# Kernel tuning notes

Hardware: AMD Instinct MI355X
Metric: run time of the kernel (lower is better)

Reference implementation:

```python
import jax, jax.numpy as jnp
import numpy as np

B, N, CIN, D, K = 8, 4096, 128, 128, 16
EPS = 1e-5


def setup_inputs() -> dict:
    key = jax.random.key(0)
    ks = jax.random.split(key, 16)
    g = lambda i, shp, s=0.05: (jax.random.normal(ks[i], shp, jnp.float32) * s)
    return {
        "xyz": jax.random.normal(ks[0], (B, N, 3), jnp.float32),
        "features": jax.random.normal(ks[1], (B, N, CIN), jnp.float32),
        # feature_transform: Linear(CIN->D) + LayerNorm(D)
        "W1": g(2, (CIN, D)), "b1": jnp.zeros((D,), jnp.float32),
        "ln1_g": jnp.ones((D,), jnp.float32), "ln1_b": jnp.zeros((D,), jnp.float32),
        # geo_encoder: Conv1d(3->D//2,1) + BN(D//2) + Conv1d(D//2->D,1)
        "cw1": g(3, (D // 2, 3), 0.3), "cb1": jnp.zeros((D // 2,), jnp.float32),
        "bn_g": jnp.ones((D // 2,), jnp.float32), "bn_b": jnp.zeros((D // 2,), jnp.float32),
        "cw2": g(4, (D, D // 2)), "cb2": jnp.zeros((D,), jnp.float32),
        # fusion: Linear(2D->D) + LayerNorm(D)
        "Wf": g(5, (2 * D, D)), "bf": jnp.zeros((D,), jnp.float32),
        "lnf_g": jnp.ones((D,), jnp.float32), "lnf_b": jnp.zeros((D,), jnp.float32),
        "alpha": jnp.ones((1, 1, D), jnp.float32), "beta": jnp.zeros((1, 1, D), jnp.float32),
    }


def _layernorm(x, g, b):
    m = x.mean(-1, keepdims=True)
    v = x.var(-1, keepdims=True)
    return (x - m) / jnp.sqrt(v + EPS) * g + b


def reference(xyz, features, W1, b1, ln1_g, ln1_b, cw1, cb1, bn_g, bn_b, cw2, cb2,
              Wf, bf, lnf_g, lnf_b, alpha, beta):
    # KNN via squared distances [B,N,N]
    sq = jnp.sum(xyz * xyz, -1)
    dist = sq[:, :, None] + sq[:, None, :] - 2.0 * jnp.einsum('bnc,bmc->bnm', xyz, xyz)
    _, idx = jax.lax.top_k(-dist, K)                       # [B,N,K] smallest dists

    gather = jax.vmap(lambda pts, i: pts[i])               # per-batch fancy gather
    nb_xyz = gather(xyz, idx)                              # [B,N,K,3]
    nb_feat = gather(features, idx)                        # [B,N,K,CIN]

    # geo encoder on relative positions (1x1 convs == per-point linear)
    rel = nb_xyz - xyz[:, :, None, :]                      # [B,N,K,3]
    h = jnp.einsum('bnkc,oc->bnko', rel, cw1) + cb1        # [B,N,K,D/2]
    mu = h.mean((0, 1, 2))                                 # BatchNorm1d (train-mode batch stats)
    var = h.var((0, 1, 2))
    h = (h - mu) / jnp.sqrt(var + EPS) * bn_g + bn_b
    h = jax.nn.silu(h)
    geo = jnp.einsum('bnkc,oc->bnko', h, cw2) + cb2        # [B,N,K,D]

    # feature transform on gathered neighbor features
    tf = jax.nn.silu(_layernorm(nb_feat @ W1 + b1, ln1_g, ln1_b))  # [B,N,K,D]

    # fuse, affine, softmax-weighted aggregation over K
    fused = jax.nn.silu(_layernorm(jnp.concatenate([tf, geo], -1) @ Wf + bf, lnf_g, lnf_b))
    fused = alpha * fused + beta                           # broadcast [1,1,D]
    w = jax.nn.softmax(fused.sum(-1), axis=-1)             # [B,N,K]
    return (w[..., None] * fused).sum(2)                   # [B,N,D]
```

## Files before the change

### kernel.cpp

```cpp
#include <hip/hip_runtime.h>
#include <hip/hip_bf16.h>

#define B_ 8
#define N_ 4096
#define K_ 16
#define D_ 128

typedef short bf16x8 __attribute__((ext_vector_type(8)));
typedef float f32x4 __attribute__((ext_vector_type(4)));

__device__ __forceinline__ short bfr(float x){
  __hip_bfloat16 h = __float2bfloat16(x);
  return *reinterpret_cast<short*>(&h);
}

__global__ __launch_bounds__(256) void prep_kernel(
    const float* __restrict__ W1, const float* __restrict__ Wf, const float* __restrict__ cw2,
    short* __restrict__ W1Tf, short* __restrict__ WfTf, short* __restrict__ cw2f,
    float* __restrict__ stats)
{
  int t = blockIdx.x*256 + threadIdx.x;
  if (t < 16384) {
    int u = t;
    int j = u & 7, L = (u >> 3) & 63, ks = (u >> 9) & 3, tt = u >> 11;
    int d = tt*16 + (L & 15);
    int c = ks*32 + (L >> 4)*8 + j;
    W1Tf[u] = bfr(W1[c*128 + d]);
  } else if (t < 49152) {
    int u = t - 16384;
    int j = u & 7, L = (u >> 3) & 63, ks = (u >> 9) & 7, tt = u >> 12;
    int d = tt*16 + (L & 15);
    int c = ks*32 + (L >> 4)*8 + j;
    WfTf[u] = bfr(Wf[c*128 + d]);
  } else if (t < 57344) {
    int u = t - 49152;
    int j = u & 7, L = (u >> 3) & 63, ks = (u >> 9) & 1, tt = u >> 10;
    int d = tt*16 + (L & 15);
    int c = ks*32 + (L >> 4)*8 + j;
    cw2f[u] = bfr(cw2[d*64 + c]);
  } else if (t < 57360) {
    stats[t - 57344] = 0.0f;
  }
}

__device__ __forceinline__ void insert16(float (&bd)[16], int (&bi)[16], float d, int cid){
  #pragma unroll
  for (int j = 15; j >= 1; --j){
    bool ltj = d < bd[j];
    bool ltp = d < bd[j-1];
    float nd = ltj ? (ltp ? bd[j-1] : d) : bd[j];
    int   ni = ltj ? (ltp ? bi[j-1] : cid) : bi[j];
    bd[j] = nd; bi[j] = ni;
  }
  bool lt0 = d < bd[0];
  bd[0] = lt0 ? d : bd[0];
  bi[0] = lt0 ? cid : bi[0];
}

__device__ __forceinline__ void insert16t(float (&bd)[16], int (&bi)[16], float d, int cid){
  bool lt[16];
  #pragma unroll
  for (int j = 0; j < 16; ++j)
    lt[j] = (d < bd[j]) || ((d == bd[j]) && (cid < bi[j]));
  #pragma unroll
  for (int j = 15; j >= 1; --j){
    float nd = lt[j] ? (lt[j-1] ? bd[j-1] : d) : bd[j];
    int   ni = lt[j] ? (lt[j-1] ? bi[j-1] : cid) : bi[j];
    bd[j] = nd; bi[j] = ni;
  }
  if (lt[0]){ bd[0] = d; bi[0] = cid; }
}

__global__ __launch_bounds__(512) void knn_split_kernel(
    const float* __restrict__ xyz,
    float* __restrict__ pd0, int* __restrict__ pi0,
    float* __restrict__ pd1, int* __restrict__ pi1)
{
  __shared__ float4 cand[2048];
  int b    = blockIdx.x >> 7;
  int h    = (blockIdx.x >> 6) & 1;
  int qblk = (blockIdx.x & 63) << 6;
  int hbase = h << 11;
  const float* xb = xyz + b*N_*3;
  for (int i = threadIdx.x; i < 2048; i += 512){
    int gi = hbase + i;
    float x = xb[gi*3+0], y = xb[gi*3+1], z = xb[gi*3+2];
    int e = i ^ ((i >> 8) & 7);
    cand[e] = make_float4(x, y, z, x*x + y*y + z*z);
  }
  __syncthreads();

  int wv = threadIdx.x >> 6, lane = threadIdx.x & 63;
  int q = lane & 7;
  int s = lane >> 3;
  int qi = qblk + (wv << 3) + q;
  const float* qp = xb + qi*3;
  float qx = qp[0], qy = qp[1], qz = qp[2];
  float4 qc = make_float4(qx, qy, qz, qx*qx + qy*qy + qz*qz);

  float bd[16]; int bi[16];
  #pragma unroll
  for (int j = 0; j < 16; ++j){ bd[j] = 3.4e38f; bi[j] = 0x7fffffff; }

  int cbase = s << 8;
  for (int m = 0; m < 256; ++m){
    float4 c = cand[cbase + (m ^ s)];
    float t = qc.x*c.x + qc.y*c.y + qc.z*c.z;
    float d = (qc.w + c.w) - 2.0f*t;
    if (d < bd[15]) insert16(bd, bi, d, cbase + m);
  }

  #pragma unroll
  for (int xm = 32; xm >= 8; xm >>= 1){
    bool absorb = (lane & xm) == 0;
    #pragma unroll
    for (int j = 0; j < 16; ++j){
      float pdj = __shfl_xor(bd[j], xm);
      int   pij = __shfl_xor(bi[j], xm);
      if (absorb) insert16t(bd, bi, pdj, pij);
    }
  }

  if (s == 0){
    int gq = b*N_ + qi;
    float* pdh = h ? pd1 : pd0;
    int*   pih = h ? pi1 : pi0;
    #pragma unroll
    for (int j = 0; j < 16; ++j){
      pdh[gq*16 + j] = bd[j];
      pih[gq*16 + j] = bi[j] + hbase;
    }
  }
}

__device__ __forceinline__ bool lexlt(float da, int ia, float db, int ib){
  return (da < db) || ((da == db) && (ia < ib));
}

__global__ __launch_bounds__(512) void knn_merge_kernel(
    const float* __restrict__ xyz,
    const float* __restrict__ pd0, const int* __restrict__ pi0,
    const float* __restrict__ pd1, const int* __restrict__ pi1,
    int* __restrict__ idx_out, float* __restrict__ stats)
{
  int gq = blockIdx.x*512 + threadIdx.x;
  int b = gq >> 12, qi = gq & 4095;

  float md[16]; int mi[16];
  #pragma unroll
  for (int i = 0; i < 16; ++i){
    float da = pd0[gq*16 + i];      int ia = pi0[gq*16 + i];
    float db = pd1[gq*16 + 15 - i]; int ib = pi1[gq*16 + 15 - i];
    bool t = lexlt(da, ia, db, ib);
    md[i] = t ? da : db; mi[i] = t ? ia : ib;
  }
  #pragma unroll
  for (int j = 8; j > 0; j >>= 1){
    #pragma unroll
    for (int i = 0; i < 16; ++i){
      int l = i ^ j;
      if (l > i){
        bool t = lexlt(md[l], mi[l], md[i], mi[i]);
        float lo_d = t ? md[l] : md[i]; int lo_i = t ? mi[l] : mi[i];
        float hi_d = t ? md[i] : md[l]; int hi_i = t ? mi[i] : mi[l];
        md[i] = lo_d; mi[i] = lo_i; md[l] = hi_d; mi[l] = hi_i;
      }
    }
  }

  const float* qp = xyz + (b*N_ + qi)*3;
  float qx = qp[0], qy = qp[1], qz = qp[2];
  float sv[9];
  #pragma unroll
  for (int i = 0; i < 9; ++i) sv[i] = 0.0f;
  #pragma unroll
  for (int j = 0; j < 16; ++j){
    idx_out[gq*16 + j] = mi[j];
    const float* np = xyz + (b*N_ + mi[j])*3;
    float rx = np[0]-qx, ry = np[1]-qy, rz = np[2]-qz;
    sv[0] += rx;    sv[1] += ry;    sv[2] += rz;
    sv[3] += rx*rx; sv[4] += ry*ry; sv[5] += rz*rz;
    sv[6] += rx*ry; sv[7] += rx*rz; sv[8] += ry*rz;
  }
  #pragma unroll
  for (int i = 0; i < 9; ++i){
    float v = sv[i];
    #pragma unroll
    for (int mask = 1; mask < 64; mask <<= 1) v += __shfl_xor(v, mask);
    if ((threadIdx.x & 63) == 0) atomicAdd(&stats[i], v);
  }
}

__global__ void bn_finalize_kernel(
    const float* __restrict__ stats, const float* __restrict__ cw1, const float* __restrict__ cb1,
    const float* __restrict__ bn_g, const float* __restrict__ bn_b,
    float* __restrict__ bnsc, float* __restrict__ bnsh)
{
  int o = threadIdx.x;
  if (o >= 64) return;
  const float inv = 1.0f / (float)(B_*N_*K_);
  float m1x = stats[0]*inv, m1y = stats[1]*inv, m1z = stats[2]*inv;
  float mxx = stats[3]*inv, myy = stats[4]*inv, mzz = stats[5]*inv;
  float mxy = stats[6]*inv, mxz = stats[7]*inv, myz = stats[8]*inv;
  float w0 = cw1[o*3], w1 = cw1[o*3+1], w2 = cw1[o*3+2], cb = cb1[o];
  float wm = w0*m1x + w1*m1y + w2*m1z;
  float mu = wm + cb;
  float e2 = w0*w0*mxx + w1*w1*myy + w2*w2*mzz
           + 2.0f*(w0*w1*mxy + w0*w2*mxz + w1*w2*myz)
           + 2.0f*cb*wm + cb*cb;
  float var = e2 - mu*mu;
  float sc = bn_g[o] * rsqrtf(var + 1e-5f);
  bnsc[o] = sc;
  bnsh[o] = bn_b[o] - mu*sc;
}

__device__ __forceinline__ void ln_silu_store(
    f32x4 (&acc)[8], const float (&pb)[8], const float (&pg)[8], const float (&pe)[8],
    short* fw, int g, int c16)
{
  float sm[4] = {0,0,0,0}, sq[4] = {0,0,0,0};
  #pragma unroll
  for (int t = 0; t < 8; ++t){
    #pragma unroll
    for (int r = 0; r < 4; ++r){
      float v = acc[t][r] + pb[t];
      acc[t][r] = v;
      sm[r] += v; sq[r] += v*v;
    }
  }
  #pragma unroll
  for (int mask = 1; mask < 16; mask <<= 1){
    #pragma unroll
    for (int r = 0; r < 4; ++r){ sm[r] += __shfl_xor(sm[r], mask); sq[r] += __shfl_xor(sq[r], mask); }
  }
  #pragma unroll
  for (int r = 0; r < 4; ++r){
    float mean = sm[r] * (1.0f/128.0f);
    float var  = sq[r]*(1.0f/128.0f) - mean*mean;
    float rstd = rsqrtf(var + 1e-5f);
    #pragma unroll
    for (int t = 0; t < 8; ++t){
      float y = (acc[t][r] - mean) * rstd * pg[t] + pe[t];
      y = y / (1.0f + __expf(-y));
      fw[(g*4 + r)*264 + t*16 + c16] = bfr(y);
    }
  }
}

__device__ __forceinline__ void geo_store(
    float rx, float ry, float rz,
    const float* s_cw1, const float* s_cb1, const float* s_sc, const float* s_sh,
    const short* __restrict__ cw2f, const float (&pc2)[8],
    short* fw, int g, int c16, int lane)
{
  bf16x8 a2[2];
  #pragma unroll
  for (int ks = 0; ks < 2; ++ks){
    bf16x8 v;
    #pragma unroll
    for (int j = 0; j < 8; ++j){
      int o = ks*32 + g*8 + j;
      float h = s_cw1[o*3]*rx + s_cw1[o*3+1]*ry + s_cw1[o*3+2]*rz + s_cb1[o];
      h = h * s_sc[o] + s_sh[o];
      h = h / (1.0f + __expf(-h));
      v[j] = bfr(h);
    }
    a2[ks] = v;
  }
  #pragma unroll
  for (int t = 0; t < 8; ++t){
    f32x4 a = (f32x4){0.f,0.f,0.f,0.f};
    #pragma unroll
    for (int ks = 0; ks < 2; ++ks){
      bf16x8 w = *(const bf16x8*)(cw2f + ((t*2 + ks)*64 + lane)*8);
      a = __builtin_amdgcn_mfma_f32_16x16x32_bf16(a2[ks], w, a, 0, 0, 0);
    }
    #pragma unroll
    for (int r = 0; r < 4; ++r)
      fw[(g*4 + r)*264 + 128 + t*16 + c16] = bfr(a[r] + pc2[t]);
  }
}

__device__ __forceinline__ void epilogue_store(
    f32x4 (&acc)[8], const float (&pbf)[8], const float (&pgf)[8], const float (&pef)[8],
    const float (&pal)[8], const float (&pbt)[8],
    int point, int g, int c16, float* __restrict__ out)
{
  float sm[4] = {0,0,0,0}, sq[4] = {0,0,0,0};
  #pragma unroll
  for (int t = 0; t < 8; ++t){
    #pragma unroll
    for (int r = 0; r < 4; ++r){
      float v = acc[t][r] + pbf[t];
      acc[t][r] = v;
      sm[r] += v; sq[r] += v*v;
    }
  }
  #pragma unroll
  for (int mask = 1; mask < 16; mask <<= 1){
    #pragma unroll
    for (int r = 0; r < 4; ++r){ sm[r] += __shfl_xor(sm[r], mask); sq[r] += __shfl_xor(sq[r], mask); }
  }
  #pragma unroll
  for (int r = 0; r < 4; ++r){
    float mean = sm[r] * (1.0f/128.0f);
    float var  = sq[r]*(1.0f/128.0f) - mean*mean;
    float rstd = rsqrtf(var + 1e-5f);
    #pragma unroll
    for (int t = 0; t < 8; ++t){
      float y = (acc[t][r] - mean) * rstd * pgf[t] + pef[t];
      y = y / (1.0f + __expf(-y));
      acc[t][r] = pal[t]*y + pbt[t];
    }
  }
  float sr[4] = {0,0,0,0};
  #pragma unroll
  for (int t = 0; t < 8; ++t){
    #pragma unroll
    for (int r = 0; r < 4; ++r) sr[r] += acc[t][r];
  }
  #pragma unroll
  for (int mask = 1; mask < 16; mask <<= 1){
    #pragma unroll
    for (int r = 0; r < 4; ++r) sr[r] += __shfl_xor(sr[r], mask);
  }
  float mx = fmaxf(fmaxf(sr[0], sr[1]), fmaxf(sr[2], sr[3]));
  mx = fmaxf(mx, __shfl_xor(mx, 16));
  mx = fmaxf(mx, __shfl_xor(mx, 32));
  float e[4]; float se = 0.f;
  #pragma unroll
  for (int r = 0; r < 4; ++r){ e[r] = __expf(sr[r] - mx); se += e[r]; }
  se += __shfl_xor(se, 16);
  se += __shfl_xor(se, 32);
  float inv = 1.0f / se;
  #pragma unroll
  for (int r = 0; r < 4; ++r) e[r] *= inv;
  #pragma unroll
  for (int t = 0; t < 8; ++t){
    float o = e[0]*acc[t][0] + e[1]*acc[t][1] + e[2]*acc[t][2] + e[3]*acc[t][3];
    o += __shfl_xor(o, 16);
    o += __shfl_xor(o, 32);
    if (g == 0) out[point*128 + t*16 + c16] = o;
  }
}

__global__ __launch_bounds__(256) void lga_main_kernel(
    const float* __restrict__ xyz, const float* __restrict__ feats, const int* __restrict__ idx_ws,
    const short* __restrict__ W1Tf, const short* __restrict__ WfTf, const short* __restrict__ cw2f,
    const float* __restrict__ b1, const float* __restrict__ ln1g, const float* __restrict__ ln1b,
    const float* __restrict__ cw1, const float* __restrict__ cb1,
    const float* __restrict__ bnsc, const float* __restrict__ bnsh,
    const float* __restrict__ cb2, const float* __restrict__ bfb,
    const float* __restrict__ lnfg, const float* __restrict__ lnfb,
    const float* __restrict__ alpha, const float* __restrict__ beta,
    float* __restrict__ out)
{
  __shared__ short fuse[4][16][264];
  __shared__ float s_cw1[192], s_cb1[64], s_sc[64], s_sh[64];

  int tid = threadIdx.x;
  for (int i = tid; i < 192; i += 256) s_cw1[i] = cw1[i];
  if (tid < 64){ s_cb1[tid] = cb1[tid]; s_sc[tid] = bnsc[tid]; s_sh[tid] = bnsh[tid]; }
  __syncthreads();

  int wv = tid >> 6, lane = tid & 63, g = lane >> 4, c16 = lane & 15;
  int point = blockIdx.x*4 + wv;
  int bb = point >> 12, n = point & 4095;

  int nb = idx_ws[point*16 + c16];
  const float* frow = feats + (bb*N_ + nb)*128;
  bf16x8 a1[4];
  #pragma unroll
  for (int ks = 0; ks < 4; ++ks){
    f32x4 lo = *(const f32x4*)(frow + ks*32 + g*8);
    f32x4 hi = *(const f32x4*)(frow + ks*32 + g*8 + 4);
    bf16x8 v;
    v[0]=bfr(lo[0]); v[1]=bfr(lo[1]); v[2]=bfr(lo[2]); v[3]=bfr(lo[3]);
    v[4]=bfr(hi[0]); v[5]=bfr(hi[1]); v[6]=bfr(hi[2]); v[7]=bfr(hi[3]);
    a1[ks] = v;
  }

  f32x4 acc[8];
  #pragma unroll
  for (int t = 0; t < 8; ++t) acc[t] = (f32x4){0.f,0.f,0.f,0.f};
  #pragma unroll
  for (int t = 0; t < 8; ++t){
    #pragma unroll
    for (int ks = 0; ks < 4; ++ks){
      bf16x8 w = *(const bf16x8*)(W1Tf + ((t*4 + ks)*64 + lane)*8);
      acc[t] = __builtin_amdgcn_mfma_f32_16x16x32_bf16(a1[ks], w, acc[t], 0, 0, 0);
    }
  }

  short* fw = &fuse[wv][0][0];
  {
    float p_b1[8], p_g1[8], p_e1[8];
    #pragma unroll
    for (int t = 0; t < 8; ++t){
      int col = t*16 + c16;
      p_b1[t] = b1[col]; p_g1[t] = ln1g[col]; p_e1[t] = ln1b[col];
    }
    ln_silu_store(acc, p_b1, p_g1, p_e1, fw, g, c16);
  }
  {
    float p_c2[8];
    #pragma unroll
    for (int t = 0; t < 8; ++t) p_c2[t] = cb2[t*16 + c16];
    const float* cx = xyz + (bb*N_ + n)*3;
    const float* nx = xyz + (bb*N_ + nb)*3;
    geo_store(nx[0]-cx[0], nx[1]-cx[1], nx[2]-cx[2],
              s_cw1, s_cb1, s_sc, s_sh, cw2f, p_c2, fw, g, c16, lane);
  }

  bf16x8 a3[8];
  #pragma unroll
  for (int ks = 0; ks < 8; ++ks)
    a3[ks] = *(const bf16x8*)(fw + c16*264 + ks*32 + g*8);

  #pragma unroll
  for (int t = 0; t < 8; ++t) acc[t] = (f32x4){0.f,0.f,0.f,0.f};
  #pragma unroll
  for (int t = 0; t < 8; ++t){
    #pragma unroll
    for (int ks = 0; ks < 8; ++ks){
      bf16x8 w = *(const bf16x8*)(WfTf + ((t*8 + ks)*64 + lane)*8);
      acc[t] = __builtin_amdgcn_mfma_f32_16x16x32_bf16(a3[ks], w, acc[t], 0, 0, 0);
    }
  }

  float p_bf[8], p_gf[8], p_ef[8], p_al[8], p_bt[8];
  #pragma unroll
  for (int t = 0; t < 8; ++t){
    int col = t*16 + c16;
    p_bf[t] = bfb[col]; p_gf[t] = lnfg[col]; p_ef[t] = lnfb[col];
    p_al[t] = alpha[col]; p_bt[t] = beta[col];
  }
  epilogue_store(acc, p_bf, p_gf, p_ef, p_al, p_bt, point, g, c16, out);
}

extern "C" void kernel_launch(void* const* d_in, const int* in_sizes, int n_in,
                              void* d_out, int out_size, void* d_ws, size_t ws_size,
                              hipStream_t stream)
{
  (void)in_sizes; (void)n_in; (void)out_size; (void)ws_size;
  const float* xyz   = (const float*)d_in[0];
  const float* feats = (const float*)d_in[1];
  const float* W1    = (const float*)d_in[2];
  const float* b1    = (const float*)d_in[3];
  const float* ln1g  = (const float*)d_in[4];
  const float* ln1b  = (const float*)d_in[5];
  const float* cw1   = (const float*)d_in[6];
  const float* cb1   = (const float*)d_in[7];
  const float* bng   = (const float*)d_in[8];
  const float* bnb   = (const float*)d_in[9];
  const float* cw2   = (const float*)d_in[10];
  const float* cb2   = (const float*)d_in[11];
  const float* Wf    = (const float*)d_in[12];
  const float* bfb   = (const float*)d_in[13];
  const float* lnfg  = (const float*)d_in[14];
  const float* lnfb  = (const float*)d_in[15];
  const float* alpha = (const float*)d_in[16];
  const float* beta  = (const float*)d_in[17];

  char* ws = (char*)d_ws;
  int*   idx   = (int*)  (ws);
  float* stats = (float*)(ws + 2097152);
  float* bnsc  = (float*)(ws + 2097216);
  float* bnsh  = (float*)(ws + 2097472);
  short* W1Tf  = (short*)(ws + 2097728);
  short* WfTf  = (short*)(ws + 2130496);
  short* cw2f  = (short*)(ws + 2196032);
  float* pd0   = (float*)(ws + 4194304);
  int*   pi0   = (int*)  (ws + 6291456);
  float* pd1   = (float*)(ws + 8388608);
  int*   pi1   = (int*)  (ws + 10485760);

  hipLaunchKernelGGL(prep_kernel, dim3(225), dim3(256), 0, stream,
                     W1, Wf, cw2, W1Tf, WfTf, cw2f, stats);
  hipLaunchKernelGGL(knn_split_kernel, dim3(1024), dim3(512), 0, stream,
                     xyz, pd0, pi0, pd1, pi1);
  hipLaunchKernelGGL(knn_merge_kernel, dim3(64), dim3(512), 0, stream,
                     xyz, pd0, pi0, pd1, pi1, idx, stats);
  hipLaunchKernelGGL(bn_finalize_kernel, dim3(1), dim3(64), 0, stream,
                     stats, cw1, cb1, bng, bnb, bnsc, bnsh);
  hipLaunchKernelGGL(lga_main_kernel, dim3(8192), dim3(256), 0, stream,
                     xyz, feats, idx, W1Tf, WfTf, cw2f,
                     b1, ln1g, ln1b, cw1, cb1, bnsc, bnsh,
                     cb2, bfb, lnfg, lnfb, alpha, beta,
                     (float*)d_out);
}
```

Measured before the change: 961.2 us.

## Split KNN candidate scan into four quarters and merge partial top-16 lists

The KNN split kernel now divides each batch's candidates into four quarters of 1024 points instead of two halves, doubling the grid to 2048 blocks and halving each thread's serial scan length. The merge kernel folds four sorted partial lists with repeated bitonic low-16 merges. Partial results are staged in the output buffer, which is later overwritten, rather than in workspace. This adds merge work and intermediate traffic in exchange for more parallelism in the distance scan.

```diff
diff --git a/kernel.cpp b/kernel.cpp
--- a/kernel.cpp
+++ b/kernel.cpp
@@ -73,19 +73,18 @@
 
 __global__ __launch_bounds__(512) void knn_split_kernel(
     const float* __restrict__ xyz,
-    float* __restrict__ pd0, int* __restrict__ pi0,
-    float* __restrict__ pd1, int* __restrict__ pi1)
-{
-  __shared__ float4 cand[2048];
-  int b    = blockIdx.x >> 7;
-  int h    = (blockIdx.x >> 6) & 1;
+    float* __restrict__ pdb, int* __restrict__ pib)
+{
+  __shared__ float4 cand[1024];
+  int b    = blockIdx.x >> 8;
+  int qtr  = (blockIdx.x >> 6) & 3;
   int qblk = (blockIdx.x & 63) << 6;
-  int hbase = h << 11;
+  int hbase = qtr << 10;
   const float* xb = xyz + b*N_*3;
-  for (int i = threadIdx.x; i < 2048; i += 512){
+  for (int i = threadIdx.x; i < 1024; i += 512){
     int gi = hbase + i;
     float x = xb[gi*3+0], y = xb[gi*3+1], z = xb[gi*3+2];
-    int e = i ^ ((i >> 8) & 7);
+    int e = i ^ ((i >> 7) & 7);
     cand[e] = make_float4(x, y, z, x*x + y*y + z*z);
   }
   __syncthreads();
@@ -102,8 +101,8 @@
   #pragma unroll
   for (int j = 0; j < 16; ++j){ bd[j] = 3.4e38f; bi[j] = 0x7fffffff; }
 
-  int cbase = s << 8;
-  for (int m = 0; m < 256; ++m){
+  int cbase = s << 7;
+  for (int m = 0; m < 128; ++m){
     float4 c = cand[cbase + (m ^ s)];
     float t = qc.x*c.x + qc.y*c.y + qc.z*c.z;
     float d = (qc.w + c.w) - 2.0f*t;
@@ -123,8 +122,8 @@
 
   if (s == 0){
     int gq = b*N_ + qi;
-    float* pdh = h ? pd1 : pd0;
-    int*   pih = h ? pi1 : pi0;
+    float* pdh = pdb + qtr*524288;
+    int*   pih = pib + qtr*524288;
     #pragma unroll
     for (int j = 0; j < 16; ++j){
       pdh[gq*16 + j] = bd[j];
@@ -137,22 +136,14 @@
   return (da < db) || ((da == db) && (ia < ib));
 }
 
-__global__ __launch_bounds__(512) void knn_merge_kernel(
-    const float* __restrict__ xyz,
-    const float* __restrict__ pd0, const int* __restrict__ pi0,
-    const float* __restrict__ pd1, const int* __restrict__ pi1,
-    int* __restrict__ idx_out, float* __restrict__ stats)
-{
-  int gq = blockIdx.x*512 + threadIdx.x;
-  int b = gq >> 12, qi = gq & 4095;
-
+__device__ __forceinline__ void low16(float (&ad)[16], int (&ai)[16],
+                                      const float (&bdv)[16], const int (&biv)[16]){
   float md[16]; int mi[16];
   #pragma unroll
   for (int i = 0; i < 16; ++i){
-    float da = pd0[gq*16 + i];      int ia = pi0[gq*16 + i];
-    float db = pd1[gq*16 + 15 - i]; int ib = pi1[gq*16 + 15 - i];
-    bool t = lexlt(da, ia, db, ib);
-    md[i] = t ? da : db; mi[i] = t ? ia : ib;
+    bool t = lexlt(ad[i], ai[i], bdv[15-i], biv[15-i]);
+    md[i] = t ? ad[i] : bdv[15-i];
+    mi[i] = t ? ai[i] : biv[15-i];
   }
   #pragma unroll
   for (int j = 8; j > 0; j >>= 1){
@@ -167,6 +158,34 @@
       }
     }
   }
+  #pragma unroll
+  for (int i = 0; i < 16; ++i){ ad[i] = md[i]; ai[i] = mi[i]; }
+}
+
+__global__ __launch_bounds__(512) void knn_merge_kernel(
+    const float* __restrict__ xyz,
+    const float* __restrict__ pdb, const int* __restrict__ pib,
+    int* __restrict__ idx_out, float* __restrict__ stats)
+{
+  int gq = blockIdx.x*512 + threadIdx.x;
+  int b = gq >> 12, qi = gq & 4095;
+
+  float ad[16]; int ai[16];
+  #pragma unroll
+  for (int j = 0; j < 16; ++j){
+    ad[j] = pdb[gq*16 + j];
+    ai[j] = pib[gq*16 + j];
+  }
+  #pragma unroll
+  for (int qtr = 1; qtr < 4; ++qtr){
+    float ld[16]; int li[16];
+    #pragma unroll
+    for (int j = 0; j < 16; ++j){
+      ld[j] = pdb[qtr*524288 + gq*16 + j];
+      li[j] = pib[qtr*524288 + gq*16 + j];
+    }
+    low16(ad, ai, ld, li);
+  }
 
   const float* qp = xyz + (b*N_ + qi)*3;
   float qx = qp[0], qy = qp[1], qz = qp[2];
@@ -175,8 +194,8 @@
   for (int i = 0; i < 9; ++i) sv[i] = 0.0f;
   #pragma unroll
   for (int j = 0; j < 16; ++j){
-    idx_out[gq*16 + j] = mi[j];
-    const float* np = xyz + (b*N_ + mi[j])*3;
+    idx_out[gq*16 + j] = ai[j];
+    const float* np = xyz + (b*N_ + ai[j])*3;
     float rx = np[0]-qx, ry = np[1]-qy, rz = np[2]-qz;
     sv[0] += rx;    sv[1] += ry;    sv[2] += rz;
     sv[3] += rx*rx; sv[4] += ry*ry; sv[5] += rz*rz;
@@ -470,17 +489,16 @@
   short* W1Tf  = (short*)(ws + 2097728);
   short* WfTf  = (short*)(ws + 2130496);
   short* cw2f  = (short*)(ws + 2196032);
-  float* pd0   = (float*)(ws + 4194304);
-  int*   pi0   = (int*)  (ws + 6291456);
-  float* pd1   = (float*)(ws + 8388608);
-  int*   pi1   = (int*)  (ws + 10485760);
+
+  float* pdb = (float*)d_out;
+  int*   pib = (int*)((char*)d_out + 8388608);
 
   hipLaunchKernelGGL(prep_kernel, dim3(225), dim3(256), 0, stream,
                      W1, Wf, cw2, W1Tf, WfTf, cw2f, stats);
-  hipLaunchKernelGGL(knn_split_kernel, dim3(1024), dim3(512), 0, stream,
-                     xyz, pd0, pi0, pd1, pi1);
+  hipLaunchKernelGGL(knn_split_kernel, dim3(2048), dim3(512), 0, stream,
+                     xyz, pdb, pib);
   hipLaunchKernelGGL(knn_merge_kernel, dim3(64), dim3(512), 0, stream,
-                     xyz, pd0, pi0, pd1, pi1, idx, stats);
+                     xyz, pdb, pib, idx, stats);
   hipLaunchKernelGGL(bn_finalize_kernel, dim3(1), dim3(64), 0, stream,
                      stats, cw1, cb1, bng, bnb, bnsc, bnsh);
   hipLaunchKernelGGL(lga_main_kernel, dim3(8192), dim3(256), 0, stream,
```

Measured after the change: 1.118 ms. 16.3% more time.
